# Performance work log

Hardware: AMD Instinct MI355X
Metric: run time of the kernel (lower is better)

The kernel has to match this reference:

```python
import jax, jax.numpy as jnp
import numpy as np

B, S, D = 4, 2048, 1024
H = 16
DH = D // H


def setup_inputs() -> dict:
    key = jax.random.key(0)
    ks = jax.random.split(key, 5)
    scale = 0.02
    return {
        "x": jax.random.normal(ks[0], (B, S, D), dtype=jnp.float32),
        "w_in": jax.random.normal(ks[1], (D, 3 * D), dtype=jnp.float32) * scale,
        "b_in": jax.random.normal(ks[2], (3 * D,), dtype=jnp.float32) * scale,
        "w_out": jax.random.normal(ks[3], (D, D), dtype=jnp.float32) * scale,
        "b_out": jax.random.normal(ks[4], (D,), dtype=jnp.float32) * scale,
        "causal_mask": 1,
    }


def reference(x, w_in, b_in, w_out, b_out, causal_mask):
    b, s, d = x.shape
    qkv = x @ w_in + b_in                       # [B,S,3D]
    q, k, v = jnp.split(qkv, 3, axis=-1)
    # [B,S,D] -> [B,H,S,DH]
    q = q.reshape(b, s, H, DH).transpose(0, 2, 1, 3)
    k = k.reshape(b, s, H, DH).transpose(0, 2, 1, 3)
    v = v.reshape(b, s, H, DH).transpose(0, 2, 1, 3)
    scores = jnp.einsum("bhqd,bhkd->bhqk", q, k)
    if causal_mask:
        # mask applied before scaling in original; -inf unaffected by scaling
        mask = jnp.triu(jnp.ones((s, s), dtype=bool), k=1)
        scores = jnp.where(mask, -jnp.inf, scores)
    scores = scores / jnp.sqrt(jnp.float32(DH))
    probs = jax.nn.softmax(scores, axis=-1)
    out = jnp.einsum("bhqk,bhkd->bhqd", probs, v)
    out = out.transpose(0, 2, 1, 3).reshape(b, s, d)
    return out @ w_out + b_out
```

## Files before the change

### kernel.cpp

```cpp
#include <hip/hip_runtime.h>
#include <hip/hip_bf16.h>
#include <cstdint>

#define NB 4
#define NS 2048
#define ND 1024
#define NH 16
#define NDH 64
#define NM (NB*NS)
#define N3D (3*ND)

typedef __attribute__((ext_vector_type(8))) short short8;
typedef __attribute__((ext_vector_type(4))) float f32x4;
typedef __attribute__((ext_vector_type(4))) unsigned short us4;
typedef __attribute__((ext_vector_type(4))) unsigned int uint4v;

__device__ __forceinline__ float bf2f(unsigned short u) {
  unsigned int i = ((unsigned int)u) << 16;
  return __builtin_bit_cast(float, i);
}
__device__ __forceinline__ unsigned short f2bf(float f) {
  unsigned int i = __builtin_bit_cast(unsigned int, f);
  i = (i + 0x7FFFu + ((i >> 16) & 1u)) >> 16;
  return (unsigned short)i;
}
__device__ __forceinline__ unsigned int cvtpk_bf16(float lo, float hi) {
  unsigned int r;
  asm("v_cvt_pk_bf16_f32 %0, %1, %2" : "=v"(r) : "v"(lo), "v"(hi));
  return r;
}

#define GLD16(g, l) __builtin_amdgcn_global_load_lds( \
    (__attribute__((address_space(1))) void*)(void*)(g), \
    (__attribute__((address_space(3))) void*)(l), 16, 0, 0)

__global__ __launch_bounds__(256) void cvt_bf16_k(
    const float* __restrict__ in, unsigned short* __restrict__ out, int n)
{
  const int i = (blockIdx.x * 256 + threadIdx.x) * 4;
  if (i + 3 < n) {
    const f32x4 v = *(const f32x4*)(in + i);
    us4 o = {f2bf(v[0]), f2bf(v[1]), f2bf(v[2]), f2bf(v[3])};
    *(us4*)(out + i) = o;
  }
}

__global__ __launch_bounds__(256) void transpose_cvt_k(
    const float* __restrict__ in, unsigned short* __restrict__ out,
    int rows, int cols)
{
  __shared__ unsigned short tile[32][33];
  const int c0 = blockIdx.x * 32, r0 = blockIdx.y * 32;
  const int tx = threadIdx.x & 31, ty = threadIdx.x >> 5;
  #pragma unroll
  for (int i = ty; i < 32; i += 8)
    tile[i][tx] = f2bf(in[(size_t)(r0 + i) * cols + (c0 + tx)]);
  __syncthreads();
  #pragma unroll
  for (int i = ty; i < 32; i += 8)
    out[(size_t)(c0 + i) * rows + (r0 + tx)] = tile[tx][i];
}

__global__ __launch_bounds__(256) void vt_transpose_k(
    const unsigned short* __restrict__ qkv, unsigned short* __restrict__ vt)
{
  __shared__ unsigned short tile[32][33];
  const int dt = blockIdx.x & 1;
  const int st = (blockIdx.x >> 1) & 63;
  const int bh = blockIdx.x >> 7;
  const int b = bh >> 4, h = bh & 15;
  const int tx = threadIdx.x & 31, ty = threadIdx.x >> 5;
  const int s0 = st * 32, d0 = dt * 32;
  const unsigned short* src = qkv + (size_t)b * NS * N3D + 2 * ND + h * NDH;
  #pragma unroll
  for (int i = ty; i < 32; i += 8)
    tile[i][tx] = src[(size_t)(s0 + i) * N3D + d0 + tx];
  __syncthreads();
  unsigned short* dst = vt + (size_t)bh * NDH * NS;
  #pragma unroll
  for (int i = ty; i < 32; i += 8)
    dst[(size_t)(d0 + i) * NS + s0 + tx] = tile[tx][i];
}

template<bool OUT_F32>
__global__ __launch_bounds__(256) void gemm_bt_bias(
    const unsigned short* __restrict__ A,
    const unsigned short* __restrict__ Bt,
    const float* __restrict__ bias,
    unsigned short* __restrict__ Cb,
    float* __restrict__ Cf,
    int M, int N, int K)
{
  __shared__ __align__(16) unsigned short Alds[128 * 32];
  __shared__ __align__(16) unsigned short Blds[128 * 32];
  const int nbn = N >> 7;
  const int nwg = (M >> 7) * nbn;
  const int cpx = nwg >> 3;
  const int tid = (blockIdx.x & 7) * cpx + (blockIdx.x >> 3);
  const int bm = tid / nbn, bn = tid % nbn;
  const int m0 = bm << 7, n0 = bn << 7;
  const int w = threadIdx.x >> 6, l = threadIdx.x & 63;
  const int wr = w >> 1, wc = w & 1;
  const int lr = l & 15, lg = l >> 4;

  const unsigned short* gA = A + (size_t)(m0 + w * 32 + (l >> 2)) * K + (l & 3) * 8;
  const unsigned short* gB = Bt + (size_t)(n0 + w * 32 + (l >> 2)) * K + (l & 3) * 8;
  unsigned short* lA = Alds + (w * 32) * 32;
  unsigned short* lB = Blds + (w * 32) * 32;

  f32x4 acc[4][4] = {};

  for (int k0 = 0; k0 < K; k0 += 32) {
    GLD16(gA + k0, lA);
    GLD16(gA + k0 + (size_t)16 * K, lA + 16 * 32);
    GLD16(gB + k0, lB);
    GLD16(gB + k0 + (size_t)16 * K, lB + 16 * 32);
    __syncthreads();

    short8 a[4], b[4];
    #pragma unroll
    for (int i = 0; i < 4; ++i)
      a[i] = *(const short8*)(Alds + (wr * 64 + i * 16 + lr) * 32 + lg * 8);
    #pragma unroll
    for (int j = 0; j < 4; ++j)
      b[j] = *(const short8*)(Blds + (wc * 64 + j * 16 + lr) * 32 + lg * 8);

    #pragma unroll
    for (int i = 0; i < 4; ++i)
      #pragma unroll
      for (int j = 0; j < 4; ++j)
        acc[i][j] = __builtin_amdgcn_mfma_f32_16x16x32_bf16(a[i], b[j], acc[i][j], 0, 0, 0);
    __syncthreads();
  }

  #pragma unroll
  for (int j = 0; j < 4; ++j) {
    const int col = n0 + wc * 64 + j * 16 + lr;
    const float bv = bias[col];
    #pragma unroll
    for (int i = 0; i < 4; ++i) {
      #pragma unroll
      for (int r = 0; r < 4; ++r) {
        const int row = m0 + wr * 64 + i * 16 + lg * 4 + r;
        const float v = acc[i][j][r] + bv;
        if (OUT_F32) Cf[(size_t)row * N + col] = v;
        else         Cb[(size_t)row * N + col] = f2bf(v);
      }
    }
  }
}

__global__ __launch_bounds__(256) void attn_fwd(
    const unsigned short* __restrict__ qkv,
    const unsigned short* __restrict__ Vt,
    unsigned short* __restrict__ out)
{
  __shared__ __align__(16) char Kl[2][64 * 128];
  __shared__ __align__(16) char Vl[2][64 * 128];

  const int bid = blockIdx.x;
  const int bh = bid & 63;
  const int slot = bid >> 6;
  const int b = bh >> 4, h = bh & 15;
  const int w = threadIdx.x >> 6, l = threadIdx.x & 63;
  const int lr = l & 15, lg = l >> 4;

  const size_t rs = N3D;
  const unsigned short* Qb = qkv + (size_t)b * NS * rs + (size_t)h * NDH;
  const unsigned short* Kb = Qb + ND;
  const unsigned short* VtB = Vt + (size_t)bh * NDH * NS;

  const int srow = l >> 3;
  const int sw = (((l & 7) * 16) ^ (srow << 4)) >> 1;
  const unsigned short* KsrcBase = Kb + (size_t)(16 * w + srow) * rs + sw;
  const unsigned short* VsrcBase = VtB + (size_t)(16 * w + srow) * NS + sw;
  const int ldsRow0 = 16 * w * 128;

  const float QSCALE = 0.125f * 1.44269504f;
  const int ksw = (lr & 7) << 4;

  #pragma unroll 1
  for (int pass = 0; pass < 2; ++pass) {
    const int qt = pass == 0 ? slot : 15 - slot;
    const int q0 = qt * 128 + w * 32;
    const int T = 2 * qt + 2;

    short8 qf[2][2];
    #pragma unroll
    for (int t = 0; t < 2; ++t) {
      const unsigned short* qrow = Qb + (size_t)(q0 + t * 16 + lr) * rs + lg * 8;
      qf[t][0] = *(const short8*)(qrow);
      qf[t][1] = *(const short8*)(qrow + 32);
      #pragma unroll
      for (int j = 0; j < 8; ++j) {
        qf[t][0][j] = (short)f2bf(bf2f((unsigned short)qf[t][0][j]) * QSCALE);
        qf[t][1][j] = (short)f2bf(bf2f((unsigned short)qf[t][1][j]) * QSCALE);
      }
    }

    float l_run[2];
    f32x4 o[2][4] = {};
    l_run[0] = l_run[1] = 0.f;

    auto stage = [&](int buf, int kt) {
      const int kb = kt << 6;
      const unsigned short* gk = KsrcBase + (size_t)kb * rs;
      GLD16(gk,          &Kl[buf][ldsRow0]);
      GLD16(gk + 8 * rs, &Kl[buf][ldsRow0 + 8 * 128]);
      const unsigned short* gv = VsrcBase + kb;
      GLD16(gv,          &Vl[buf][ldsRow0]);
      GLD16(gv + 8 * NS, &Vl[buf][ldsRow0 + 8 * 128]);
    };

    stage(0, 0);
    __syncthreads();

    #pragma unroll 1
    for (int kt = 0; kt < T; ++kt) {
      const int cur = kt & 1;
      if (kt + 1 < T) stage(cur ^ 1, kt + 1);
      const int kbase = kt << 6;

      if (kbase <= q0 + 31) {
        short8 kf[4][2];
        #pragma unroll
        for (int ks = 0; ks < 4; ++ks) {
          const char* rowp = &Kl[cur][(ks * 16 + lr) * 128];
          kf[ks][0] = *(const short8*)(rowp + ((lg * 16) ^ ksw));
          kf[ks][1] = *(const short8*)(rowp + ((64 + lg * 16) ^ ksw));
        }

        f32x4 s[4][2] = {};
        #pragma unroll
        for (int ks = 0; ks < 4; ++ks)
          #pragma unroll
          for (int t = 0; t < 2; ++t) {
            s[ks][t] = __builtin_amdgcn_mfma_f32_16x16x32_bf16(kf[ks][0], qf[t][0], s[ks][t], 0, 0, 0);
            s[ks][t] = __builtin_amdgcn_mfma_f32_16x16x32_bf16(kf[ks][1], qf[t][1], s[ks][t], 0, 0, 0);
          }

        short8 vf[4][2];
        #pragma unroll
        for (int nb = 0; nb < 4; ++nb) {
          const char* rowp = &Vl[cur][(nb * 16 + lr) * 128];
          vf[nb][0] = *(const short8*)(rowp + ((lg * 16) ^ ksw));
          vf[nb][1] = *(const short8*)(rowp + ((64 + lg * 16) ^ ksw));
        }

        const bool domask = (kbase + 63 > q0);
        #pragma unroll
        for (int t = 0; t < 2; ++t) {
          const int qi = q0 + t * 16 + lr;
          float p[16];
          if (domask) {
            #pragma unroll
            for (int ks = 0; ks < 4; ++ks)
              #pragma unroll
              for (int r = 0; r < 4; ++r)
                p[ks * 4 + r] = (kbase + ks * 16 + lg * 4 + r > qi)
                                  ? 0.f : exp2f(s[ks][t][r]);
          } else {
            #pragma unroll
            for (int ks = 0; ks < 4; ++ks)
              #pragma unroll
              for (int r = 0; r < 4; ++r)
                p[ks * 4 + r] = exp2f(s[ks][t][r]);
          }
          float s0 = (p[0] + p[1]) + (p[2] + p[3]);
          float s1 = (p[4] + p[5]) + (p[6] + p[7]);
          float s2 = (p[8] + p[9]) + (p[10] + p[11]);
          float s3 = (p[12] + p[13]) + (p[14] + p[15]);
          l_run[t] += (s0 + s1) + (s2 + s3);

          unsigned A0 = cvtpk_bf16(p[0],  p[1]),  B0 = cvtpk_bf16(p[2],  p[3]);
          unsigned A1 = cvtpk_bf16(p[4],  p[5]),  B1 = cvtpk_bf16(p[6],  p[7]);
          unsigned A2 = cvtpk_bf16(p[8],  p[9]),  B2 = cvtpk_bf16(p[10], p[11]);
          unsigned A3 = cvtpk_bf16(p[12], p[13]), B3 = cvtpk_bf16(p[14], p[15]);

          asm("v_permlane32_swap_b32 %0, %1" : "+v"(A0), "+v"(A1));
          asm("v_permlane16_swap_b32 %0, %1" : "+v"(A0), "+v"(A1));
          asm("v_permlane32_swap_b32 %0, %1" : "+v"(B0), "+v"(B1));
          asm("v_permlane16_swap_b32 %0, %1" : "+v"(B0), "+v"(B1));
          asm("v_permlane32_swap_b32 %0, %1" : "+v"(A2), "+v"(A3));
          asm("v_permlane16_swap_b32 %0, %1" : "+v"(A2), "+v"(A3));
          asm("v_permlane32_swap_b32 %0, %1" : "+v"(B2), "+v"(B3));
          asm("v_permlane16_swap_b32 %0, %1" : "+v"(B2), "+v"(B3));

          uint4v u0 = {A0, B0, A1, B1};
          uint4v u1 = {A2, B2, A3, B3};
          short8 pf0 = __builtin_bit_cast(short8, u0);
          short8 pf1 = __builtin_bit_cast(short8, u1);

          #pragma unroll
          for (int nb = 0; nb < 4; ++nb)
            o[t][nb] = __builtin_amdgcn_mfma_f32_16x16x32_bf16(pf0, vf[nb][0], o[t][nb], 0, 0, 0);
          #pragma unroll
          for (int nb = 0; nb < 4; ++nb)
            o[t][nb] = __builtin_amdgcn_mfma_f32_16x16x32_bf16(pf1, vf[nb][1], o[t][nb], 0, 0, 0);
        }
      }

      __syncthreads();
    }

    #pragma unroll
    for (int t = 0; t < 2; ++t) {
      float lt = l_run[t];
      lt += __shfl_xor(lt, 16);
      lt += __shfl_xor(lt, 32);
      #pragma unroll
      for (int rr = 0; rr < 4; ++rr) {
        const float lq = __shfl(lt, lg * 4 + rr);
        const float inv = 1.0f / lq;
        const int qi = q0 + t * 16 + lg * 4 + rr;
        #pragma unroll
        for (int nb = 0; nb < 4; ++nb)
          out[(size_t)(b * NS + qi) * ND + h * NDH + nb * 16 + lr] = f2bf(o[t][nb][rr] * inv);
      }
    }
  }
}

extern "C" void kernel_launch(void* const* d_in, const int* in_sizes, int n_in,
                              void* d_out, int out_size, void* d_ws, size_t ws_size,
                              hipStream_t stream) {
  const float* x     = (const float*)d_in[0];
  const float* w_in  = (const float*)d_in[1];
  const float* b_in  = (const float*)d_in[2];
  const float* w_out = (const float*)d_in[3];
  const float* b_out = (const float*)d_in[4];
  float* out = (float*)d_out;

  char* ws = (char*)d_ws;
  size_t off = 0;
  unsigned short* x_bf    = (unsigned short*)(ws + off); off += (size_t)NM * ND * 2;
  unsigned short* qkv     = (unsigned short*)(ws + off); off += (size_t)NM * N3D * 2;
  unsigned short* attn    = (unsigned short*)(ws + off); off += (size_t)NM * ND * 2;
  unsigned short* w_in_t  = (unsigned short*)(ws + off); off += (size_t)N3D * ND * 2;
  unsigned short* w_out_t = (unsigned short*)(ws + off); off += (size_t)ND * ND * 2;
  unsigned short* vt = x_bf;

  cvt_bf16_k<<<dim3((NM * ND) / (256 * 4)), 256, 0, stream>>>(x, x_bf, NM * ND);
  transpose_cvt_k<<<dim3(N3D / 32, ND / 32), 256, 0, stream>>>(w_in, w_in_t, ND, N3D);
  transpose_cvt_k<<<dim3(ND / 32, ND / 32), 256, 0, stream>>>(w_out, w_out_t, ND, ND);

  gemm_bt_bias<false><<<dim3((NM / 128) * (N3D / 128)), 256, 0, stream>>>(
      x_bf, w_in_t, b_in, qkv, nullptr, NM, N3D, ND);

  vt_transpose_k<<<dim3(64 * 64 * 2), 256, 0, stream>>>(qkv, vt);

  attn_fwd<<<dim3(64 * 8), 256, 0, stream>>>(qkv, vt, attn);

  gemm_bt_bias<true><<<dim3((NM / 128) * (ND / 128)), 256, 0, stream>>>(
      attn, w_out_t, b_out, nullptr, out, NM, ND, ND);
}
```

Baseline: 215.8 us.

## Halve attention query tile to 64 rows and double grid size

The attention kernel now gives each workgroup 64-row query tiles instead of 128, so each wave owns 16 query rows rather than 32. Pairing is now chunk c with 31-c, and the grid doubles to 1024 blocks. The aim is more parallelism and better load balance across CUs, and it also drops the per-tile causal skip branch. In exchange, each K/V tile loaded into LDS is reused by half as many query rows, so total K/V traffic roughly doubles and there is less MFMA work per barrier.

New measurement: 210.0 us. -2.7%, faster.

```diff
diff --git a/kernel.cpp b/kernel.cpp
--- a/kernel.cpp
+++ b/kernel.cpp
@@ -181,26 +181,24 @@
 
   #pragma unroll 1
   for (int pass = 0; pass < 2; ++pass) {
-    const int qt = pass == 0 ? slot : 15 - slot;
-    const int q0 = qt * 128 + w * 32;
-    const int T = 2 * qt + 2;
-
-    short8 qf[2][2];
-    #pragma unroll
-    for (int t = 0; t < 2; ++t) {
-      const unsigned short* qrow = Qb + (size_t)(q0 + t * 16 + lr) * rs + lg * 8;
-      qf[t][0] = *(const short8*)(qrow);
-      qf[t][1] = *(const short8*)(qrow + 32);
+    const int c = pass == 0 ? slot : 31 - slot;
+    const int q0 = c * 64 + w * 16;
+    const int T = c + 1;
+
+    short8 qf[2];
+    {
+      const unsigned short* qrow = Qb + (size_t)(q0 + lr) * rs + lg * 8;
+      qf[0] = *(const short8*)(qrow);
+      qf[1] = *(const short8*)(qrow + 32);
       #pragma unroll
       for (int j = 0; j < 8; ++j) {
-        qf[t][0][j] = (short)f2bf(bf2f((unsigned short)qf[t][0][j]) * QSCALE);
-        qf[t][1][j] = (short)f2bf(bf2f((unsigned short)qf[t][1][j]) * QSCALE);
+        qf[0][j] = (short)f2bf(bf2f((unsigned short)qf[0][j]) * QSCALE);
+        qf[1][j] = (short)f2bf(bf2f((unsigned short)qf[1][j]) * QSCALE);
       }
     }
 
-    float l_run[2];
-    f32x4 o[2][4] = {};
-    l_run[0] = l_run[1] = 0.f;
+    float l_run = 0.f;
+    f32x4 o[4] = {};
 
     auto stage = [&](int buf, int kt) {
       const int kb = kt << 6;
@@ -221,101 +219,93 @@
       if (kt + 1 < T) stage(cur ^ 1, kt + 1);
       const int kbase = kt << 6;
 
-      if (kbase <= q0 + 31) {
-        short8 kf[4][2];
-        #pragma unroll
-        for (int ks = 0; ks < 4; ++ks) {
-          const char* rowp = &Kl[cur][(ks * 16 + lr) * 128];
-          kf[ks][0] = *(const short8*)(rowp + ((lg * 16) ^ ksw));
-          kf[ks][1] = *(const short8*)(rowp + ((64 + lg * 16) ^ ksw));
-        }
-
-        f32x4 s[4][2] = {};
+      short8 kf[4][2];
+      #pragma unroll
+      for (int ks = 0; ks < 4; ++ks) {
+        const char* rowp = &Kl[cur][(ks * 16 + lr) * 128];
+        kf[ks][0] = *(const short8*)(rowp + ((lg * 16) ^ ksw));
+        kf[ks][1] = *(const short8*)(rowp + ((64 + lg * 16) ^ ksw));
+      }
+
+      f32x4 s[4] = {};
+      #pragma unroll
+      for (int ks = 0; ks < 4; ++ks) {
+        s[ks] = __builtin_amdgcn_mfma_f32_16x16x32_bf16(kf[ks][0], qf[0], s[ks], 0, 0, 0);
+        s[ks] = __builtin_amdgcn_mfma_f32_16x16x32_bf16(kf[ks][1], qf[1], s[ks], 0, 0, 0);
+      }
+
+      short8 vf[4][2];
+      #pragma unroll
+      for (int nb = 0; nb < 4; ++nb) {
+        const char* rowp = &Vl[cur][(nb * 16 + lr) * 128];
+        vf[nb][0] = *(const short8*)(rowp + ((lg * 16) ^ ksw));
+        vf[nb][1] = *(const short8*)(rowp + ((64 + lg * 16) ^ ksw));
+      }
+
+      const bool domask = (kbase + 63 > q0);
+      const int qi = q0 + lr;
+      float p[16];
+      if (domask) {
         #pragma unroll
         for (int ks = 0; ks < 4; ++ks)
           #pragma unroll
-          for (int t = 0; t < 2; ++t) {
-            s[ks][t] = __builtin_amdgcn_mfma_f32_16x16x32_bf16(kf[ks][0], qf[t][0], s[ks][t], 0, 0, 0);
-            s[ks][t] = __builtin_amdgcn_mfma_f32_16x16x32_bf16(kf[ks][1], qf[t][1], s[ks][t], 0, 0, 0);
-          }
-
-        short8 vf[4][2];
+          for (int r = 0; r < 4; ++r)
+            p[ks * 4 + r] = (kbase + ks * 16 + lg * 4 + r > qi)
+                              ? 0.f : exp2f(s[ks][r]);
+      } else {
         #pragma unroll
-        for (int nb = 0; nb < 4; ++nb) {
-          const char* rowp = &Vl[cur][(nb * 16 + lr) * 128];
-          vf[nb][0] = *(const short8*)(rowp + ((lg * 16) ^ ksw));
-          vf[nb][1] = *(const short8*)(rowp + ((64 + lg * 16) ^ ksw));
-        }
-
-        const bool domask = (kbase + 63 > q0);
-        #pragma unroll
-        for (int t = 0; t < 2; ++t) {
-          const int qi = q0 + t * 16 + lr;
-          float p[16];
-          if (domask) {
-            #pragma unroll
-            for (int ks = 0; ks < 4; ++ks)
-              #pragma unroll
-              for (int r = 0; r < 4; ++r)
-                p[ks * 4 + r] = (kbase + ks * 16 + lg * 4 + r > qi)
-                                  ? 0.f : exp2f(s[ks][t][r]);
-          } else {
-            #pragma unroll
-            for (int ks = 0; ks < 4; ++ks)
-              #pragma unroll
-              for (int r = 0; r < 4; ++r)
-                p[ks * 4 + r] = exp2f(s[ks][t][r]);
-          }
-          float s0 = (p[0] + p[1]) + (p[2] + p[3]);
-          float s1 = (p[4] + p[5]) + (p[6] + p[7]);
-          float s2 = (p[8] + p[9]) + (p[10] + p[11]);
-          float s3 = (p[12] + p[13]) + (p[14] + p[15]);
-          l_run[t] += (s0 + s1) + (s2 + s3);
-
-          unsigned A0 = cvtpk_bf16(p[0],  p[1]),  B0 = cvtpk_bf16(p[2],  p[3]);
-          unsigned A1 = cvtpk_bf16(p[4],  p[5]),  B1 = cvtpk_bf16(p[6],  p[7]);
-          unsigned A2 = cvtpk_bf16(p[8],  p[9]),  B2 = cvtpk_bf16(p[10], p[11]);
-          unsigned A3 = cvtpk_bf16(p[12], p[13]), B3 = cvtpk_bf16(p[14], p[15]);
-
-          asm("v_permlane32_swap_b32 %0, %1" : "+v"(A0), "+v"(A1));
-          asm("v_permlane16_swap_b32 %0, %1" : "+v"(A0), "+v"(A1));
-          asm("v_permlane32_swap_b32 %0, %1" : "+v"(B0), "+v"(B1));
-          asm("v_permlane16_swap_b32 %0, %1" : "+v"(B0), "+v"(B1));
-          asm("v_permlane32_swap_b32 %0, %1" : "+v"(A2), "+v"(A3));
-          asm("v_permlane16_swap_b32 %0, %1" : "+v"(A2), "+v"(A3));
-          asm("v_permlane32_swap_b32 %0, %1" : "+v"(B2), "+v"(B3));
-          asm("v_permlane16_swap_b32 %0, %1" : "+v"(B2), "+v"(B3));
-
-          uint4v u0 = {A0, B0, A1, B1};
-          uint4v u1 = {A2, B2, A3, B3};
-          short8 pf0 = __builtin_bit_cast(short8, u0);
-          short8 pf1 = __builtin_bit_cast(short8, u1);
-
+        for (int ks = 0; ks < 4; ++ks)
           #pragma unroll
-          for (int nb = 0; nb < 4; ++nb)
-            o[t][nb] = __builtin_amdgcn_mfma_f32_16x16x32_bf16(pf0, vf[nb][0], o[t][nb], 0, 0, 0);
-          #pragma unroll
-          for (int nb = 0; nb < 4; ++nb)
-            o[t][nb] = __builtin_amdgcn_mfma_f32_16x16x32_bf16(pf1, vf[nb][1], o[t][nb], 0, 0, 0);
-        }
-      }
+          for (int r = 0; r < 4; ++r)
+            p[ks * 4 + r] = exp2f(s[ks][r]);
+      }
+      float s0 = (p[0] + p[1]) + (p[2] + p[3]);
+      float s1 = (p[4] + p[5]) + (p[6] + p[7]);
+      float s2 = (p[8] + p[9]) + (p[10] + p[11]);
+      float s3 = (p[12] + p[13]) + (p[14] + p[15]);
+      l_run += (s0 + s1) + (s2 + s3);
+
+      unsigned A0 = cvtpk_bf16(p[0],  p[1]),  B0 = cvtpk_bf16(p[2],  p[3]);
+      unsigned A1 = cvtpk_bf16(p[4],  p[5]),  B1 = cvtpk_bf16(p[6],  p[7]);
+      unsigned A2 = cvtpk_bf16(p[8],  p[9]),  B2 = cvtpk_bf16(p[10], p[11]);
+      unsigned A3 = cvtpk_bf16(p[12], p[13]), B3 = cvtpk_bf16(p[14], p[15]);
+
+      asm("v_permlane32_swap_b32 %0, %1" : "+v"(A0), "+v"(A1));
+      asm("v_permlane16_swap_b32 %0, %1" : "+v"(A0), "+v"(A1));
+      asm("v_permlane32_swap_b32 %0, %1" : "+v"(B0), "+v"(B1));
+      asm("v_permlane16_swap_b32 %0, %1" : "+v"(B0), "+v"(B1));
+      asm("v_permlane32_swap_b32 %0, %1" : "+v"(A2), "+v"(A3));
+      asm("v_permlane16_swap_b32 %0, %1" : "+v"(A2), "+v"(A3));
+      asm("v_permlane32_swap_b32 %0, %1" : "+v"(B2), "+v"(B3));
+      asm("v_permlane16_swap_b32 %0, %1" : "+v"(B2), "+v"(B3));
+
+      uint4v u0 = {A0, B0, A1, B1};
+      uint4v u1 = {A2, B2, A3, B3};
+      short8 pf0 = __builtin_bit_cast(short8, u0);
+      short8 pf1 = __builtin_bit_cast(short8, u1);
+
+      #pragma unroll
+      for (int nb = 0; nb < 4; ++nb)
+        o[nb] = __builtin_amdgcn_mfma_f32_16x16x32_bf16(pf0, vf[nb][0], o[nb], 0, 0, 0);
+      #pragma unroll
+      for (int nb = 0; nb < 4; ++nb)
+        o[nb] = __builtin_amdgcn_mfma_f32_16x16x32_bf16(pf1, vf[nb][1], o[nb], 0, 0, 0);
 
       __syncthreads();
     }
 
-    #pragma unroll
-    for (int t = 0; t < 2; ++t) {
-      float lt = l_run[t];
+    {
+      float lt = l_run;
       lt += __shfl_xor(lt, 16);
       lt += __shfl_xor(lt, 32);
       #pragma unroll
       for (int rr = 0; rr < 4; ++rr) {
         const float lq = __shfl(lt, lg * 4 + rr);
         const float inv = 1.0f / lq;
-        const int qi = q0 + t * 16 + lg * 4 + rr;
+        const int qi = q0 + lg * 4 + rr;
         #pragma unroll
         for (int nb = 0; nb < 4; ++nb)
-          out[(size_t)(b * NS + qi) * ND + h * NDH + nb * 16 + lr] = f2bf(o[t][nb][rr] * inv);
+          out[(size_t)(b * NS + qi) * ND + h * NDH + nb * 16 + lr] = f2bf(o[nb][rr] * inv);
       }
     }
   }
@@ -349,7 +339,7 @@
 
   vt_transpose_k<<<dim3(64 * 64 * 2), 256, 0, stream>>>(qkv, vt);
 
-  attn_fwd<<<dim3(64 * 8), 256, 0, stream>>>(qkv, vt, attn);
+  attn_fwd<<<dim3(64 * 16), 256, 0, stream>>>(qkv, vt, attn);
 
   gemm_bt_bias<true><<<dim3((NM / 128) * (ND / 128)), 256, 0, stream>>>(
       attn, w_out_t, b_out, nullptr, out, NM, ND, ND);
```
